# Optimization experiments

Measured on AMD Instinct MI355X. Metric: run time of the kernel, lower is better.

Reference implementation:

```python
import jax, jax.numpy as jnp
import numpy as np

TEMPERATURE = 0.07
LOG_EPS = 1e-20
MEAN_EPS = 1e-6


def setup_inputs() -> dict:
    key = jax.random.key(0)
    k1, k2, k3 = jax.random.split(key, 3)
    B, T1, I1, C = 64, 33, 197, 512  # 1+seqlen=33, 1+14*14=197
    text_embeds = jax.random.normal(k1, (B, T1, C), dtype=jnp.float32)
    video_embeds = jax.random.normal(k2, (B, I1, C), dtype=jnp.float32)
    text_attn_mask = jax.random.randint(k3, (B, T1), 0, 2).astype(jnp.int32)
    # guarantee every row has at least one attended (non-CLS) token
    text_attn_mask = text_attn_mask.at[:, :2].set(1)
    return {"text_embeds": text_embeds, "video_embeds": video_embeds,
            "text_attn_mask": text_attn_mask}


def reference(text_embeds, video_embeds, text_attn_mask):
    # NOTE: original normalizes over dim=1 (sequence axis), kept faithfully.
    te = text_embeds / jnp.linalg.norm(text_embeds, axis=1, keepdims=True)
    ve = video_embeds / jnp.linalg.norm(video_embeds, axis=1, keepdims=True)
    mask = text_attn_mask[:, 1:].astype(bool)          # [B, T] (trim CLS)
    text_latents = te[:, 1:, :]                        # [B, T, C]
    # full late-interaction score tensor, scaled (multiplied) by temperature
    sim = jnp.einsum('xtd,yid->xyti', text_latents, ve) * TEMPERATURE  # [X,Y,T,I]

    # text -> image: max over image tokens, masked mean over text tokens
    t2i = sim.max(axis=-1)                             # [X, Y, T]
    m = mask[None, :, None, :]                         # [1, B, 1, T] (X must == B)
    numer = jnp.where(m, t2i[None], 0.0).sum(axis=-1)  # [1, B, Y]
    denom = jnp.maximum(mask.sum(axis=-1).astype(sim.dtype), MEAN_EPS)[None, :, None]
    text_to_image = numer / denom                      # [1, B, Y]

    # image -> text: masked max over text tokens, mean over image tokens
    # (computed in the original module but unused in the returned loss)
    m5 = mask[None, :, None, :, None]                  # [1, B, 1, T, 1]
    neg = -jnp.finfo(sim.dtype).max
    image_to_text = jnp.where(m5, sim[None], neg).max(axis=-2).mean(axis=-1)  # [1,B,Y]
    del image_to_text  # dead in original: loss = text_to_image_loss only

    t2i_exp = jnp.exp(text_to_image)                   # [1, B, Y]
    pos = jnp.diagonal(t2i_exp, axis1=-2, axis2=-1)    # [1, min(B, Y)]
    den = t2i_exp.sum(axis=-1)                         # [1, B]
    loss = -jnp.log(pos / den + LOG_EPS).mean(axis=-1)  # [1]
    return loss
```

## Files before the change

kernel.cpp:

```cpp
#include <hip/hip_runtime.h>
#include <hip/hip_bf16.h>
#include <float.h>
#include <math.h>

#define BB 64
#define T1 33
#define TT 32
#define II 197
#define CC 512
#define TEMP 0.07f

typedef float f32x4 __attribute__((ext_vector_type(4)));
typedef int i32x4 __attribute__((ext_vector_type(4)));
typedef int i32x8 __attribute__((ext_vector_type(8)));

#define TL_OFF  0
#define VE_OFF  (1 << 20)
#define TTI_OFF ((1 << 20) + (8 << 20))
#define KS_STRIDE   32768
#define GRP_STRIDE  131072

__global__ __launch_bounds__(512) void norm_all_kernel(const float* __restrict__ text,
                                                       const float* __restrict__ video,
                                                       unsigned char* __restrict__ tl8,
                                                       unsigned char* __restrict__ ve8) {
  int b = blockIdx.x, hz = blockIdx.y, tid = threadIdx.x;
  bool isV = hz < 4;
  int h2 = isV ? hz : hz - 4;
  const float* src = isV ? (video + (size_t)b * II * CC) : (text + (size_t)b * T1 * CC);
  int n = isV ? II : T1;

  __shared__ float cache[II][132];
  __shared__ float red[16][128];
  __shared__ float rn[128];

  {
    int c4 = tid & 31, rg = tid >> 5;
    const float* p = src + h2 * 128 + c4 * 4;
    float4 s = {0.f, 0.f, 0.f, 0.f};
    for (int i = rg; i < n; i += 16) {
      float4 v = *(const float4*)(p + (size_t)i * CC);
      *(float4*)&cache[i][c4 * 4] = v;
      s.x += v.x * v.x; s.y += v.y * v.y; s.z += v.z * v.z; s.w += v.w * v.w;
    }
    *(float4*)&red[rg][c4 * 4] = s;
  }
  __syncthreads();
  if (tid < 128) {
    float s = 0.f;
#pragma unroll
    for (int g = 0; g < 16; ++g) s += red[g][tid];
    rn[tid] = 1.0f / sqrtf(s);
  }
  __syncthreads();

  if (isV) {
    for (int S = tid; S < 13 * 128; S += 512) {
      int fb = S >> 7, h = (S >> 6) & 1, lane = S & 63;
      int i = fb * 16 + (lane & 15);
      int kloc = ((lane >> 4) & 3) * 32 + h * 16;
      unsigned int wd[4];
#pragma unroll
      for (int q = 0; q < 4; ++q) {
        f32x4 u = {0.f, 0.f, 0.f, 0.f};
        if (i < II) u = *(const f32x4*)&cache[i][kloc + q * 4];
        f32x4 r = *(const f32x4*)&rn[kloc + q * 4];
        int wv = __builtin_amdgcn_cvt_pk_fp8_f32(u[0] * r[0], u[1] * r[1], 0, 0);
        wv = __builtin_amdgcn_cvt_pk_fp8_f32(u[2] * r[2], u[3] * r[3], wv, 1);
        wd[q] = (unsigned int)wv;
      }
      unsigned char* dst = ve8 + (size_t)b * GRP_STRIDE + h2 * KS_STRIDE +
                           fb * 2048 + h * 1024 + lane * 16;
      *(uint4*)dst = make_uint4(wd[0], wd[1], wd[2], wd[3]);
    }
  } else if (tid < 256) {
    int fa_local = tid >> 7, h = (tid >> 6) & 1, lane = tid & 63;
    int t = fa_local * 16 + (lane & 15);
    int kloc = ((lane >> 4) & 3) * 32 + h * 16;
    unsigned int wd[4];
#pragma unroll
    for (int q = 0; q < 4; ++q) {
      f32x4 u = *(const f32x4*)&cache[1 + t][kloc + q * 4];
      f32x4 r = *(const f32x4*)&rn[kloc + q * 4];
      int wv = __builtin_amdgcn_cvt_pk_fp8_f32(u[0] * r[0], u[1] * r[1], 0, 0);
      wv = __builtin_amdgcn_cvt_pk_fp8_f32(u[2] * r[2], u[3] * r[3], wv, 1);
      wd[q] = (unsigned int)wv;
    }
    int fa = (b & 7) * 2 + fa_local;
    unsigned char* dst = tl8 + (size_t)(b >> 3) * GRP_STRIDE + h2 * KS_STRIDE +
                         fa * 2048 + h * 1024 + lane * 16;
    *(uint4*)dst = make_uint4(wd[0], wd[1], wd[2], wd[3]);
  }
}

typedef __attribute__((address_space(3))) unsigned int lds_u32;
typedef __attribute__((address_space(1))) const unsigned int glb_u32;
__device__ __forceinline__ void gl16(const unsigned char* g, unsigned char* l) {
  __builtin_amdgcn_global_load_lds((glb_u32*)(const void*)g, (lds_u32*)(void*)l, 16, 0, 0);
}

__global__ __launch_bounds__(512, 4) void sim_kernel(const unsigned char* __restrict__ tl8,
                                                     const unsigned char* __restrict__ ve8,
                                                     const int* __restrict__ mask,
                                                     float* __restrict__ tti) {
  int L = blockIdx.x;
  int xcd = L & 7;
  int idx = L >> 3;
  int y = xcd * 8 + (idx & 7);
  int xcb = idx >> 3;

  int tid = threadIdx.x;
  int w = tid >> 6, lane = tid & 63;
  int wm = w >> 2;
  int wn = w & 3;

  __shared__ __attribute__((aligned(16))) unsigned char As[2][4 * 2048];
  __shared__ __attribute__((aligned(16))) unsigned char Bs[2][13 * 2048];
  float* smax = (float*)&As[0][0];

  const unsigned char* Abase =
      tl8 + (size_t)(xcb >> 2) * GRP_STRIDE + (size_t)(xcb & 3) * 4 * 2048;
  const unsigned char* Bbase = ve8 + (size_t)y * GRP_STRIDE;

#define STG(s_) do {                                                          \
    int slot_ = (s_) & 1;                                                     \
    _Pragma("unroll")                                                         \
    for (int r_ = 0; r_ < 5; ++r_) {                                          \
      int u_ = w * 5 + r_;                                                    \
      if (u_ < 8) {                                                           \
        int fa_ = u_ >> 1, h_ = u_ & 1;                                       \
        const unsigned char* src_ =                                           \
            Abase + (size_t)(s_) * KS_STRIDE + fa_ * 2048 + h_ * 1024 + lane * 16; \
        gl16(src_, &As[slot_][(fa_ * 2 + h_) * 1024 + lane * 16]);            \
      } else if (u_ < 34) {                                                   \
        int gb_ = u_ - 8;                                                     \
        int fb_ = gb_ >> 1, h_ = gb_ & 1;                                     \
        const unsigned char* src_ =                                           \
            Bbase + (size_t)(s_) * KS_STRIDE + fb_ * 2048 + h_ * 1024 + lane * 16; \
        gl16(src_, &Bs[slot_][(fb_ * 2 + h_) * 1024 + lane * 16]);            \
      }                                                                       \
    }                                                                         \
  } while (0)

#define KCOMPUTE(slot_) do {                                                  \
    i32x8 aop_[2];                                                            \
    _Pragma("unroll")                                                         \
    for (int ma_ = 0; ma_ < 2; ++ma_) {                                       \
      i32x4 h0_ = *(const i32x4*)&As[slot_][((wm * 2 + ma_) * 2) * 1024 + lane * 16]; \
      i32x4 h1_ = *(const i32x4*)&As[slot_][((wm * 2 + ma_) * 2 + 1) * 1024 + lane * 16]; \
      aop_[ma_] = __builtin_shufflevector(h0_, h1_, 0, 1, 2, 3, 4, 5, 6, 7);  \
    }                                                                         \
    __builtin_amdgcn_s_setprio(1);                                            \
    _Pragma("unroll")                                                         \
    for (int nb_ = 0; nb_ < 3; ++nb_) {                                       \
      int fb_ = wn + 4 * nb_;                                                 \
      i32x4 h0_ = *(const i32x4*)&Bs[slot_][(fb_ * 2) * 1024 + lane * 16];    \
      i32x4 h1_ = *(const i32x4*)&Bs[slot_][(fb_ * 2 + 1) * 1024 + lane * 16]; \
      i32x8 bop_ = __builtin_shufflevector(h0_, h1_, 0, 1, 2, 3, 4, 5, 6, 7); \
      _Pragma("unroll")                                                       \
      for (int ma_ = 0; ma_ < 2; ++ma_)                                       \
        acc[ma_][nb_] = __builtin_amdgcn_mfma_scale_f32_16x16x128_f8f6f4(     \
            aop_[ma_], bop_, acc[ma_][nb_], 0, 0,                             \
            0, 0x7F7F7F7F, 0, 0x7F7F7F7F);                                    \
    }                                                                         \
    if (wn == 0) {                                                            \
      i32x4 h0_ = *(const i32x4*)&Bs[slot_][(12 * 2) * 1024 + lane * 16];     \
      i32x4 h1_ = *(const i32x4*)&Bs[slot_][(12 * 2 + 1) * 1024 + lane * 16]; \
      i32x8 bop_ = __builtin_shufflevector(h0_, h1_, 0, 1, 2, 3, 4, 5, 6, 7); \
      _Pragma("unroll")                                                       \
      for (int ma_ = 0; ma_ < 2; ++ma_)                                       \
        acc[ma_][3] = __builtin_amdgcn_mfma_scale_f32_16x16x128_f8f6f4(       \
            aop_[ma_], bop_, acc[ma_][3], 0, 0,                               \
            0, 0x7F7F7F7F, 0, 0x7F7F7F7F);                                    \
    }                                                                         \
    __builtin_amdgcn_s_setprio(0);                                            \
  } while (0)

  f32x4 acc[2][4] = {};

  STG(0);
  asm volatile("s_waitcnt vmcnt(0)" ::: "memory");
  __builtin_amdgcn_s_barrier();

  STG(1);
  KCOMPUTE(0);
  asm volatile("s_waitcnt vmcnt(0)" ::: "memory");
  __builtin_amdgcn_s_barrier();
  STG(2);
  KCOMPUTE(1);
  asm volatile("s_waitcnt vmcnt(0)" ::: "memory");
  __builtin_amdgcn_s_barrier();
  STG(3);
  KCOMPUTE(0);
  asm volatile("s_waitcnt vmcnt(0)" ::: "memory");
  __builtin_amdgcn_s_barrier();
  KCOMPUTE(1);
#undef STG
#undef KCOMPUTE

  int col = lane & 15, gq = lane >> 4;
  int nfrag = (wn == 0) ? 4 : 3;
  bool valid[4];
#pragma unroll
  for (int nb = 0; nb < 4; ++nb) {
    int fb = wn + 4 * nb;
    valid[nb] = (nb < nfrag) && (fb * 16 + col < II);
  }

  float mx[2][4];
#pragma unroll
  for (int ma = 0; ma < 2; ++ma)
#pragma unroll
    for (int reg = 0; reg < 4; ++reg) {
      float m = -FLT_MAX;
#pragma unroll
      for (int nb = 0; nb < 4; ++nb)
        if (valid[nb]) m = fmaxf(m, acc[ma][nb][reg]);
      mx[ma][reg] = m;
    }
#pragma unroll
  for (int st = 1; st <= 8; st <<= 1)
#pragma unroll
    for (int ma = 0; ma < 2; ++ma)
#pragma unroll
      for (int reg = 0; reg < 4; ++reg)
        mx[ma][reg] = fmaxf(mx[ma][reg], __shfl_xor(mx[ma][reg], st));

  __syncthreads();
  if (col == 0) {
#pragma unroll
    for (int ma = 0; ma < 2; ++ma)
#pragma unroll
      for (int reg = 0; reg < 4; ++reg)
        smax[wn * 64 + wm * 32 + ma * 16 + gq * 4 + reg] = mx[ma][reg];
  }
  __syncthreads();

  if (tid < 64) {
    int r = tid;
    float m = fmaxf(fmaxf(smax[r], smax[64 + r]),
                    fmaxf(smax[128 + r], smax[192 + r]));
    int x = xcb * 2 + (r >> 5), tt = r & 31;
    int mk = mask[x * T1 + 1 + tt];
    float num = mk ? m * TEMP : 0.f;
    float cnt = mk ? 1.f : 0.f;
#pragma unroll
    for (int st = 1; st < 32; st <<= 1) {
      num += __shfl_xor(num, st);
      cnt += __shfl_xor(cnt, st);
    }
    if (tt == 0) tti[x * 64 + y] = num / fmaxf(cnt, 1e-6f);
  }
}

__global__ void loss_kernel(const float* __restrict__ tti, float* __restrict__ out) {
  __shared__ float lxs[64];
  int tid = threadIdx.x;
  int x = tid >> 4, q = tid & 15;
  float4 v = *(const float4*)&tti[x * 64 + q * 4];
  float den = expf(v.x) + expf(v.y) + expf(v.z) + expf(v.w);
#pragma unroll
  for (int st = 1; st < 16; st <<= 1) den += __shfl_xor(den, st);
  if (q == 0) {
    float pos = expf(tti[x * 64 + x]);
    lxs[x] = -logf(pos / den + 1e-20f);
  }
  __syncthreads();
  if (tid < 64) {
    float lx = lxs[tid];
#pragma unroll
    for (int s = 1; s < 64; s <<= 1) lx += __shfl_xor(lx, s);
    if (tid == 0) out[0] = lx * (1.0f / 64.0f);
  }
}

extern "C" void kernel_launch(void* const* d_in, const int* in_sizes, int n_in,
                              void* d_out, int out_size, void* d_ws, size_t ws_size,
                              hipStream_t stream) {
  const float* text = (const float*)d_in[0];
  const float* video = (const float*)d_in[1];
  const int* mask = (const int*)d_in[2];
  float* out = (float*)d_out;

  char* ws = (char*)d_ws;
  unsigned char* tl8 = (unsigned char*)(ws + TL_OFF);
  unsigned char* ve8 = (unsigned char*)(ws + VE_OFF);
  float* tti = (float*)(ws + TTI_OFF);

  hipLaunchKernelGGL(norm_all_kernel, dim3(BB, 8), dim3(512), 0, stream, text, video, tl8, ve8);
  hipLaunchKernelGGL(sim_kernel, dim3(2048), dim3(512), 0, stream, tl8, ve8, mask, tti);
  hipLaunchKernelGGL(loss_kernel, dim3(1), dim3(1024), 0, stream, tti, out);
}
```

Before: 44.00 us.

## Load MFMA operands directly from global memory instead of LDS staging

Removes the double-buffered LDS staging (global_load_lds plus barriers) in the FP8 MFMA similarity kernel. Each wave now reads its A and B fragments straight from global memory in a simple k-loop. The warp mapping also changes from wm=w>>2 / wn=w&3 to wm=w&1 / wn=w>>1. This drops the LDS footprint and the per-stage barriers, but operands shared across waves are fetched redundantly from L2/global, and the removed software pipeline means load latency is no longer overlapped explicitly.

```diff
diff --git a/kernel.cpp b/kernel.cpp
--- a/kernel.cpp
+++ b/kernel.cpp
@@ -93,12 +93,6 @@
   }
 }
 
-typedef __attribute__((address_space(3))) unsigned int lds_u32;
-typedef __attribute__((address_space(1))) const unsigned int glb_u32;
-__device__ __forceinline__ void gl16(const unsigned char* g, unsigned char* l) {
-  __builtin_amdgcn_global_load_lds((glb_u32*)(const void*)g, (lds_u32*)(void*)l, 16, 0, 0);
-}
-
 __global__ __launch_bounds__(512, 4) void sim_kernel(const unsigned char* __restrict__ tl8,
                                                      const unsigned char* __restrict__ ve8,
                                                      const int* __restrict__ mask,
@@ -111,92 +105,56 @@
 
   int tid = threadIdx.x;
   int w = tid >> 6, lane = tid & 63;
-  int wm = w >> 2;
-  int wn = w & 3;
-
-  __shared__ __attribute__((aligned(16))) unsigned char As[2][4 * 2048];
-  __shared__ __attribute__((aligned(16))) unsigned char Bs[2][13 * 2048];
-  float* smax = (float*)&As[0][0];
+  int wm = w & 1;
+  int wn = w >> 1;
+
+  __shared__ float smax[4 * 64];
 
   const unsigned char* Abase =
       tl8 + (size_t)(xcb >> 2) * GRP_STRIDE + (size_t)(xcb & 3) * 4 * 2048;
   const unsigned char* Bbase = ve8 + (size_t)y * GRP_STRIDE;
 
-#define STG(s_) do {                                                          \
-    int slot_ = (s_) & 1;                                                     \
-    _Pragma("unroll")                                                         \
-    for (int r_ = 0; r_ < 5; ++r_) {                                          \
-      int u_ = w * 5 + r_;                                                    \
-      if (u_ < 8) {                                                           \
-        int fa_ = u_ >> 1, h_ = u_ & 1;                                       \
-        const unsigned char* src_ =                                           \
-            Abase + (size_t)(s_) * KS_STRIDE + fa_ * 2048 + h_ * 1024 + lane * 16; \
-        gl16(src_, &As[slot_][(fa_ * 2 + h_) * 1024 + lane * 16]);            \
-      } else if (u_ < 34) {                                                   \
-        int gb_ = u_ - 8;                                                     \
-        int fb_ = gb_ >> 1, h_ = gb_ & 1;                                     \
-        const unsigned char* src_ =                                           \
-            Bbase + (size_t)(s_) * KS_STRIDE + fb_ * 2048 + h_ * 1024 + lane * 16; \
-        gl16(src_, &Bs[slot_][(fb_ * 2 + h_) * 1024 + lane * 16]);            \
-      }                                                                       \
-    }                                                                         \
-  } while (0)
-
-#define KCOMPUTE(slot_) do {                                                  \
-    i32x8 aop_[2];                                                            \
-    _Pragma("unroll")                                                         \
-    for (int ma_ = 0; ma_ < 2; ++ma_) {                                       \
-      i32x4 h0_ = *(const i32x4*)&As[slot_][((wm * 2 + ma_) * 2) * 1024 + lane * 16]; \
-      i32x4 h1_ = *(const i32x4*)&As[slot_][((wm * 2 + ma_) * 2 + 1) * 1024 + lane * 16]; \
-      aop_[ma_] = __builtin_shufflevector(h0_, h1_, 0, 1, 2, 3, 4, 5, 6, 7);  \
-    }                                                                         \
-    __builtin_amdgcn_s_setprio(1);                                            \
-    _Pragma("unroll")                                                         \
-    for (int nb_ = 0; nb_ < 3; ++nb_) {                                       \
-      int fb_ = wn + 4 * nb_;                                                 \
-      i32x4 h0_ = *(const i32x4*)&Bs[slot_][(fb_ * 2) * 1024 + lane * 16];    \
-      i32x4 h1_ = *(const i32x4*)&Bs[slot_][(fb_ * 2 + 1) * 1024 + lane * 16]; \
-      i32x8 bop_ = __builtin_shufflevector(h0_, h1_, 0, 1, 2, 3, 4, 5, 6, 7); \
-      _Pragma("unroll")                                                       \
-      for (int ma_ = 0; ma_ < 2; ++ma_)                                       \
-        acc[ma_][nb_] = __builtin_amdgcn_mfma_scale_f32_16x16x128_f8f6f4(     \
-            aop_[ma_], bop_, acc[ma_][nb_], 0, 0,                             \
-            0, 0x7F7F7F7F, 0, 0x7F7F7F7F);                                    \
-    }                                                                         \
-    if (wn == 0) {                                                            \
-      i32x4 h0_ = *(const i32x4*)&Bs[slot_][(12 * 2) * 1024 + lane * 16];     \
-      i32x4 h1_ = *(const i32x4*)&Bs[slot_][(12 * 2 + 1) * 1024 + lane * 16]; \
-      i32x8 bop_ = __builtin_shufflevector(h0_, h1_, 0, 1, 2, 3, 4, 5, 6, 7); \
-      _Pragma("unroll")                                                       \
-      for (int ma_ = 0; ma_ < 2; ++ma_)                                       \
-        acc[ma_][3] = __builtin_amdgcn_mfma_scale_f32_16x16x128_f8f6f4(       \
-            aop_[ma_], bop_, acc[ma_][3], 0, 0,                               \
-            0, 0x7F7F7F7F, 0, 0x7F7F7F7F);                                    \
-    }                                                                         \
-    __builtin_amdgcn_s_setprio(0);                                            \
-  } while (0)
-
   f32x4 acc[2][4] = {};
 
-  STG(0);
-  asm volatile("s_waitcnt vmcnt(0)" ::: "memory");
-  __builtin_amdgcn_s_barrier();
-
-  STG(1);
-  KCOMPUTE(0);
-  asm volatile("s_waitcnt vmcnt(0)" ::: "memory");
-  __builtin_amdgcn_s_barrier();
-  STG(2);
-  KCOMPUTE(1);
-  asm volatile("s_waitcnt vmcnt(0)" ::: "memory");
-  __builtin_amdgcn_s_barrier();
-  STG(3);
-  KCOMPUTE(0);
-  asm volatile("s_waitcnt vmcnt(0)" ::: "memory");
-  __builtin_amdgcn_s_barrier();
-  KCOMPUTE(1);
-#undef STG
-#undef KCOMPUTE
+#pragma unroll 1
+  for (int s = 0; s < 4; ++s) {
+    const unsigned char* ab = Abase + (size_t)s * KS_STRIDE + lane * 16;
+    const unsigned char* bb = Bbase + (size_t)s * KS_STRIDE + lane * 16;
+
+    i32x8 aop[2];
+#pragma unroll
+    for (int ma = 0; ma < 2; ++ma) {
+      const unsigned char* p = ab + (wm * 2 + ma) * 2048;
+      i32x4 h0 = *(const i32x4*)p;
+      i32x4 h1 = *(const i32x4*)(p + 1024);
+      aop[ma] = __builtin_shufflevector(h0, h1, 0, 1, 2, 3, 4, 5, 6, 7);
+    }
+
+#pragma unroll
+    for (int nb = 0; nb < 3; ++nb) {
+      int fb = wn + 4 * nb;
+      const unsigned char* p = bb + fb * 2048;
+      i32x4 h0 = *(const i32x4*)p;
+      i32x4 h1 = *(const i32x4*)(p + 1024);
+      i32x8 bop = __builtin_shufflevector(h0, h1, 0, 1, 2, 3, 4, 5, 6, 7);
+#pragma unroll
+      for (int ma = 0; ma < 2; ++ma)
+        acc[ma][nb] = __builtin_amdgcn_mfma_scale_f32_16x16x128_f8f6f4(
+            aop[ma], bop, acc[ma][nb], 0, 0,
+            0, 0x7F7F7F7F, 0, 0x7F7F7F7F);
+    }
+    if (wn == 0) {
+      const unsigned char* p = bb + 12 * 2048;
+      i32x4 h0 = *(const i32x4*)p;
+      i32x4 h1 = *(const i32x4*)(p + 1024);
+      i32x8 bop = __builtin_shufflevector(h0, h1, 0, 1, 2, 3, 4, 5, 6, 7);
+#pragma unroll
+      for (int ma = 0; ma < 2; ++ma)
+        acc[ma][3] = __builtin_amdgcn_mfma_scale_f32_16x16x128_f8f6f4(
+            aop[ma], bop, acc[ma][3], 0, 0,
+            0, 0x7F7F7F7F, 0, 0x7F7F7F7F);
+    }
+  }
 
   int col = lane & 15, gq = lane >> 4;
   int nfrag = (wn == 0) ? 4 : 3;
@@ -226,7 +184,6 @@
       for (int reg = 0; reg < 4; ++reg)
         mx[ma][reg] = fmaxf(mx[ma][reg], __shfl_xor(mx[ma][reg], st));
 
-  __syncthreads();
   if (col == 0) {
 #pragma unroll
     for (int ma = 0; ma < 2; ++ma)
```

Measured after the change: 41.88 us, median of 2. 1.05x faster.
